# Optimization experiments

Measured on AMD Instinct MI355X. Metric: run time of the kernel, lower is better.

The kernel has to match this reference:

```python
import jax, jax.numpy as jnp
import numpy as np
import math

IN_C, N_EMBD, HEADS = 256, 512, 8

def setup_inputs() -> dict:
    key = jax.random.key(0)
    ks = jax.random.split(key, 5)
    B, T = 64, 500
    x = jax.random.normal(ks[0], (B, T, IN_C), dtype=jnp.float32)
    # torch Linear: y = x @ W.T + b; store W as [out, in]
    w_attn = jax.random.normal(ks[1], (3 * N_EMBD, IN_C), dtype=jnp.float32) * (1.0 / math.sqrt(IN_C))
    b_attn = jax.random.normal(ks[2], (3 * N_EMBD,), dtype=jnp.float32) * 0.02
    w_proj = jax.random.normal(ks[3], (N_EMBD, N_EMBD), dtype=jnp.float32) * (1.0 / math.sqrt(N_EMBD))
    b_proj = jax.random.normal(ks[4], (N_EMBD,), dtype=jnp.float32) * 0.02
    return {"x": x, "w_attn": w_attn, "b_attn": b_attn, "w_proj": w_proj, "b_proj": b_proj}

def reference(x, w_attn, b_attn, w_proj, b_proj):
    B, T, C = x.shape
    H, D = HEADS, N_EMBD // HEADS
    qkv = jnp.einsum('btc,ec->bte', x, w_attn) + b_attn  # [B,T,3*n_embd]
    q, k, v = jnp.split(qkv, 3, axis=-1)
    # [B,T,n_embd] -> [B,H,T,D]
    q = q.reshape(B, T, H, D).transpose(0, 2, 1, 3)
    k = k.reshape(B, T, H, D).transpose(0, 2, 1, 3)
    v = v.reshape(B, T, H, D).transpose(0, 2, 1, 3)
    att = jnp.einsum('bhtd,bhsd->bhts', q, k) * (1.0 / math.sqrt(D))
    # bias buffer is all-ones: masked_fill(bias==0, -inf) is a no-op
    att = jax.nn.softmax(att, axis=-1)
    y = jnp.einsum('bhts,bhsd->bhtd', att, v)  # [B,H,T,D]
    y = y.transpose(0, 2, 1, 3).reshape(B, T, N_EMBD)
    return jnp.einsum('bte,fe->btf', y, w_proj) + b_proj
```

## Files before the change

kernel.cpp:

```cpp
#include <hip/hip_runtime.h>

typedef _Float16 f16;
typedef _Float16 f16x8 __attribute__((ext_vector_type(8)));
typedef _Float16 f16x4 __attribute__((ext_vector_type(4)));
typedef _Float16 f16x2 __attribute__((ext_vector_type(2)));
typedef float    f32x16 __attribute__((ext_vector_type(16)));
typedef unsigned int u32;

typedef const __attribute__((address_space(1))) void GVOID;
typedef __attribute__((address_space(3))) void LVOID;

static __device__ __forceinline__ f32x16 mfma32(f16x8 a, f16x8 b, f32x16 c) {
  return __builtin_amdgcn_mfma_f32_32x32x16_f16(a, b, c, 0, 0, 0);
}
static __device__ __forceinline__ void gl_lds16(const f16* g, f16* l) {
  __builtin_amdgcn_global_load_lds((GVOID*)g, (LVOID*)l, 16, 0, 0);
}
static __device__ __forceinline__ u32 pk(float a, float b) {
  union { f16x2 h; u32 w; } u;
  u.h[0] = (f16)a; u.h[1] = (f16)b;
  return u.w;
}
static __device__ __forceinline__ u32 pkh(f16 a, f16 b) {
  union { f16x2 h; u32 w; } u;
  u.h[0] = a; u.h[1] = b;
  return u.w;
}
static __device__ __forceinline__ f16x8 mkfrag(float a0, float a1, float a2, float a3,
                                               float a4, float a5, float a6, float a7) {
  u32 c01 = pk(a0, a1), c23 = pk(a2, a3), c45 = pk(a4, a5), c67 = pk(a6, a7);
  asm("v_permlane32_swap_b32 %0, %1" : "+v"(c01), "+v"(c45));
  asm("v_permlane32_swap_b32 %0, %1" : "+v"(c23), "+v"(c67));
  union { f16x8 h; u32 w[4]; } u;
  u.w[0] = c01; u.w[1] = c23; u.w[2] = c45; u.w[3] = c67;
  return u.h;
}

__global__ __launch_bounds__(256)
void cvt_all(const float* __restrict__ x,  f16* __restrict__ xh,
             const float* __restrict__ wa, f16* __restrict__ wah,
             const float* __restrict__ wp, f16* __restrict__ wph) {
  int i = (blockIdx.x * 256 + threadIdx.x) * 8;
  const float* s; f16* d;
  if (i < 8192000)            { s = x + i;                 d = xh + i; }
  else if (i < 8192000+393216){ int j = i - 8192000;       s = wa + j; d = wah + j; }
  else                        { int j = i - 8585216;       s = wp + j; d = wph + j; }
  float4 v0 = *(const float4*)(s);
  float4 v1 = *(const float4*)(s + 4);
  f16x8 h;
  h[0] = (f16)v0.x; h[1] = (f16)v0.y; h[2] = (f16)v0.z; h[3] = (f16)v0.w;
  h[4] = (f16)v1.x; h[5] = (f16)v1.y; h[6] = (f16)v1.z; h[7] = (f16)v1.w;
  *(f16x8*)d = h;
}

template<int EPI, int KD, int NDIM>
__global__ __launch_bounds__(512)
void gemmdb(const f16* __restrict__ A, const f16* __restrict__ B,
            const float* __restrict__ bias, f16* __restrict__ outH,
            float* __restrict__ outF) {
  constexpr int KT = KD / 64;
  constexpr int ABUF = 128 * 64, BUFSZ = 2 * ABUF;
  __shared__ __align__(16) f16 lds[2 * BUFSZ];

  const int nwg = gridDim.x, orig = blockIdx.x;
  const int xcd = orig & 7, loc = orig >> 3;
  const int qq = nwg >> 3, rr8 = nwg & 7;
  const int gb = (xcd < rr8 ? xcd * (qq + 1) : rr8 * (qq + 1) + (xcd - rr8) * qq) + loc;
  constexpr int NB = NDIM / 128;
  const int mb = gb / NB, nb = gb - mb * NB;
  const int m0 = mb * 128, n0 = nb * 128;

  const int tid = threadIdx.x, wid = tid >> 6;
  const int l31 = tid & 31, hi = (tid >> 5) & 1;
  const int wm = (wid >> 2) * 64, wn = (wid & 3) * 32;

  f32x16 acc[2] = {};

  const int c0 = tid, c1 = 512 + tid;
  const int r0 = c0 >> 3, col0 = 8 * ((c0 & 7) ^ (r0 & 7));
  const int r1 = c1 >> 3, col1 = 8 * ((c1 & 7) ^ (r1 & 7));

  auto STAGE = [&](int t, int bufi) {
    const int k0 = t * 64;
    f16* Ab = &lds[bufi * BUFSZ];
    f16* Bb = Ab + ABUF;
    gl_lds16(A + (size_t)(m0 + r0) * KD + k0 + col0, &Ab[c0 * 8]);
    gl_lds16(A + (size_t)(m0 + r1) * KD + k0 + col1, &Ab[c1 * 8]);
    gl_lds16(B + (size_t)(n0 + r0) * KD + k0 + col0, &Bb[c0 * 8]);
    gl_lds16(B + (size_t)(n0 + r1) * KD + k0 + col1, &Bb[c1 * 8]);
  };

  STAGE(0, 0);
  int cur = 0;
#pragma unroll
  for (int t = 0; t < KT; ++t) {
    if (t + 1 < KT) {
      STAGE(t + 1, cur ^ 1);
      asm volatile("s_waitcnt vmcnt(4)" ::: "memory");
    } else {
      asm volatile("s_waitcnt vmcnt(0)" ::: "memory");
    }
    __builtin_amdgcn_sched_barrier(0);
    __builtin_amdgcn_s_barrier();

    const f16* Ab = &lds[cur * BUFSZ];
    const f16* Bb = Ab + ABUF;
    __builtin_amdgcn_s_setprio(1);
#pragma unroll
    for (int kk = 0; kk < 4; ++kk) {
      int rb = wn + l31;
      f16x8 bf = *(const f16x8*)&Bb[rb * 64 + 8 * ((2 * kk + hi) ^ (rb & 7))];
      int ra0 = wm + l31, ra1 = wm + 32 + l31;
      f16x8 af0 = *(const f16x8*)&Ab[ra0 * 64 + 8 * ((2 * kk + hi) ^ (ra0 & 7))];
      f16x8 af1 = *(const f16x8*)&Ab[ra1 * 64 + 8 * ((2 * kk + hi) ^ (ra1 & 7))];
      acc[0] = mfma32(af0, bf, acc[0]);
      acc[1] = mfma32(af1, bf, acc[1]);
    }
    __builtin_amdgcn_s_setprio(0);
    __builtin_amdgcn_s_barrier();
    cur ^= 1;
  }

  float bv = bias[n0 + wn + l31];
#pragma unroll
  for (int ms = 0; ms < 2; ++ms)
#pragma unroll
    for (int r = 0; r < 16; ++r) {
      int mrow = (r & 3) + 8 * (r >> 2) + 4 * hi;
      int m_g = m0 + wm + ms * 32 + mrow;
      int n_g = n0 + wn + l31;
      float v = acc[ms][r] + bv;
      if (EPI == 0) outH[(size_t)m_g * NDIM + n_g] = (f16)v;
      else          outF[(size_t)m_g * NDIM + n_g] = v;
    }
}

__global__ __launch_bounds__(512, 4)
void attn_kern(const f16* __restrict__ qkv, f16* __restrict__ Yg) {
  __shared__ __align__(16) f16 Kl[2][64 * 64];
  __shared__ __align__(16) f16 VT[2][64 * 64];
  const int id = blockIdx.x;
  const int g = (id & 7) * 128 + (id >> 3);
  const int bh = g >> 1, qt = g & 1;
  const int b = bh >> 3, h = bh & 7;
  const int tid = threadIdx.x, w = tid >> 6;
  const int l31 = tid & 31, hi = (tid & 63) >> 5, e7 = l31 & 7;

  const f16* base  = qkv + (size_t)b * 500 * 1536 + h * 64;
  const f16* Kbase = base + 512;
  const f16* Vbase = base + 1024;

  const int q = qt * 256 + w * 32 + l31;
  const int qc = q < 500 ? q : 499;
  f16x8 qf[4];
  const f16* qp = base + (size_t)qc * 1536 + hi * 8;
#pragma unroll
  for (int ds = 0; ds < 4; ++ds) qf[ds] = *(const f16x8*)(qp + 16 * ds);
  const f16 qs = (f16)(0.125f * 1.44269504f);
#pragma unroll
  for (int ds = 0; ds < 4; ++ds)
#pragma unroll
    for (int j = 0; j < 8; ++j) qf[ds][j] *= qs;

  f32x16 O0 = {}, O1 = {};
  float l = 0.f;

  const int krow = tid >> 3, kcol = 8 * ((tid & 7) ^ (krow & 7));
  const int kvp = (tid & 31) * 2, d4 = (tid >> 5) * 4;
  f16x4 va, vb;
  const f16x4 VZ4 = {};

  {
    gl_lds16(Kbase + (size_t)krow * 1536 + kcol, &Kl[0][tid * 8]);
    const f16* vp0 = Vbase + (size_t)kvp * 1536 + d4;
    va = *(const f16x4*)vp0; vb = *(const f16x4*)(vp0 + 1536);
#pragma unroll
    for (int dd = 0; dd < 4; ++dd) {
      int d = d4 + dd;
      *(u32*)&VT[0][d * 64 + (kvp ^ ((d & 7) << 3))] = pkh(va[dd], vb[dd]);
    }
    __syncthreads();
  }

#pragma unroll 2
  for (int kt = 0; kt < 8; ++kt) {
    const int cur = kt & 1, nxt = cur ^ 1;
    if (kt < 7) {
      const int kvn = (kt + 1) * 64;
      int kr = kvn + krow; kr = kr < 500 ? kr : 499;
      gl_lds16(Kbase + (size_t)kr * 1536 + kcol, &Kl[nxt][tid * 8]);
      int kv = kvn + kvp;
      int kc0 = kv < 500 ? kv : 499, kc1 = kv + 1 < 500 ? kv + 1 : 499;
      va = *(const f16x4*)(Vbase + (size_t)kc0 * 1536 + d4);
      vb = *(const f16x4*)(Vbase + (size_t)kc1 * 1536 + d4);
      if (kv >= 500) va = VZ4;
      if (kv + 1 >= 500) vb = VZ4;
    }

    f32x16 s0 = {}, s1 = {};
    __builtin_amdgcn_s_setprio(1);
#pragma unroll
    for (int ds = 0; ds < 4; ++ds) {
      f16x8 k0 = *(const f16x8*)&Kl[cur][l31 * 64 + 8 * ((hi + 2 * ds) ^ e7)];
      f16x8 k1 = *(const f16x8*)&Kl[cur][(32 + l31) * 64 + 8 * ((hi + 2 * ds) ^ e7)];
      s0 = mfma32(k0, qf[ds], s0);
      s1 = mfma32(k1, qf[ds], s1);
    }
    __builtin_amdgcn_s_setprio(0);

    if (kt == 7) {
#pragma unroll
      for (int r = 0; r < 16; ++r) {
        int kvL = (r & 3) + 8 * (r >> 2) + 4 * hi;
        if (480 + kvL >= 500) s1[r] = -1e30f;
      }
    }

    float ps = 0.f;
#pragma unroll
    for (int r = 0; r < 16; ++r) {
      float t = __builtin_amdgcn_exp2f(s0[r]);
      s0[r] = t; ps += t;
    }
#pragma unroll
    for (int r = 0; r < 16; ++r) {
      float t = __builtin_amdgcn_exp2f(s1[r]);
      s1[r] = t; ps += t;
    }
    ps += __shfl_xor(ps, 32);
    l += ps;

    f16x8 pf0 = mkfrag(s0[0], s0[1], s0[2], s0[3], s0[4], s0[5], s0[6], s0[7]);
    f16x8 pf1 = mkfrag(s0[8], s0[9], s0[10], s0[11], s0[12], s0[13], s0[14], s0[15]);
    f16x8 pf2 = mkfrag(s1[0], s1[1], s1[2], s1[3], s1[4], s1[5], s1[6], s1[7]);
    f16x8 pf3 = mkfrag(s1[8], s1[9], s1[10], s1[11], s1[12], s1[13], s1[14], s1[15]);

    __builtin_amdgcn_s_setprio(1);
#pragma unroll
    for (int ks = 0; ks < 4; ++ks) {
      f16x8 pf = ks == 0 ? pf0 : ks == 1 ? pf1 : ks == 2 ? pf2 : pf3;
      int sw = (16 * ks + 8 * hi) ^ (e7 << 3);
      f16x8 v0 = *(const f16x8*)&VT[cur][l31 * 64 + sw];
      f16x8 v1 = *(const f16x8*)&VT[cur][(32 + l31) * 64 + sw];
      O0 = mfma32(pf, v0, O0);
      O1 = mfma32(pf, v1, O1);
    }
    __builtin_amdgcn_s_setprio(0);

    if (kt < 7) {
#pragma unroll
      for (int dd = 0; dd < 4; ++dd) {
        int d = d4 + dd;
        *(u32*)&VT[nxt][d * 64 + (kvp ^ ((d & 7) << 3))] = pkh(va[dd], vb[dd]);
      }
    }
    __syncthreads();
  }

  float linv = __builtin_amdgcn_rcpf(l);
#pragma unroll
  for (int r = 0; r < 16; ++r) {
    int rowv = (r & 3) + 8 * (r >> 2) + 4 * hi;
    float li = __shfl(linv, rowv);
    int t = qt * 256 + w * 32 + rowv;
    if (t < 500) {
      size_t rowb = (size_t)(b * 500 + t) * 512 + h * 64;
      Yg[rowb + l31]      = (f16)(O0[r] * li);
      Yg[rowb + 32 + l31] = (f16)(O1[r] * li);
    }
  }
}

extern "C" void kernel_launch(void* const* d_in, const int* in_sizes, int n_in,
                              void* d_out, int out_size, void* d_ws, size_t ws_size,
                              hipStream_t stream) {
  const float* x      = (const float*)d_in[0];
  const float* w_attn = (const float*)d_in[1];
  const float* b_attn = (const float*)d_in[2];
  const float* w_proj = (const float*)d_in[3];
  const float* b_proj = (const float*)d_in[4];
  float* out = (float*)d_out;

  char* wsp = (char*)d_ws;
  f16* Yg   = (f16*)wsp;
  f16* x_h  = (f16*)wsp;
  f16* qkv  = (f16*)(wsp + 32768000);
  f16* wa_h = (f16*)(wsp + 32768000 + 98304000);
  f16* wp_h = (f16*)(wsp + 32768000 + 98304000 + 786432);
  if (ws_size < 132382720) return;

  cvt_all<<<4320, dim3(256), 0, stream>>>(x, x_h, w_attn, wa_h, w_proj, wp_h);

  gemmdb<0, 256, 1536><<<3000, dim3(512), 0, stream>>>(x_h, wa_h, b_attn, qkv, nullptr);
  attn_kern<<<1024, dim3(512), 0, stream>>>(qkv, Yg);
  gemmdb<1, 512, 512><<<1000, dim3(512), 0, stream>>>(Yg, wp_h, b_proj, nullptr, out);
}
```

Measured before the change: 137.7 us.

## Fuse fp32-to-fp16 input conversion into QKV GEMM with larger M tiles

Drops the separate pass that converted x to fp16. The QKV projection GEMM now loads fp32 x directly through registers, converts it while writing to LDS, and uses 256x128 tiles with register-staged double buffering in place of global_load_lds. This removes one full read and write of the fp16 copy of x plus a launch. In exchange the GEMM reads twice the A bytes and loses the asynchronous direct-to-LDS loads, and its epilogue stores scalar f16 values.

New measurement: 159.2 us. 1.16x slower.

```diff
diff --git a/kernel.cpp b/kernel.cpp
--- a/kernel.cpp
+++ b/kernel.cpp
@@ -37,20 +37,142 @@
 }
 
 __global__ __launch_bounds__(256)
-void cvt_all(const float* __restrict__ x,  f16* __restrict__ xh,
-             const float* __restrict__ wa, f16* __restrict__ wah,
-             const float* __restrict__ wp, f16* __restrict__ wph) {
+void cvt_w(const float* __restrict__ wa, f16* __restrict__ wah,
+           const float* __restrict__ wp, f16* __restrict__ wph) {
   int i = (blockIdx.x * 256 + threadIdx.x) * 8;
   const float* s; f16* d;
-  if (i < 8192000)            { s = x + i;                 d = xh + i; }
-  else if (i < 8192000+393216){ int j = i - 8192000;       s = wa + j; d = wah + j; }
-  else                        { int j = i - 8585216;       s = wp + j; d = wph + j; }
+  if (i < 393216) { s = wa + i; d = wah + i; }
+  else            { int j = i - 393216; s = wp + j; d = wph + j; }
   float4 v0 = *(const float4*)(s);
   float4 v1 = *(const float4*)(s + 4);
   f16x8 h;
   h[0] = (f16)v0.x; h[1] = (f16)v0.y; h[2] = (f16)v0.z; h[3] = (f16)v0.w;
   h[4] = (f16)v1.x; h[5] = (f16)v1.y; h[6] = (f16)v1.z; h[7] = (f16)v1.w;
   *(f16x8*)d = h;
+}
+
+__global__ __launch_bounds__(512)
+void gemm1f(const float* __restrict__ A, const f16* __restrict__ B,
+            const float* __restrict__ bias, f16* __restrict__ outH) {
+  constexpr int KD = 256, KT = 4, NB = 12;
+  constexpr int ABUF = 256 * 64, BBUF = 128 * 64, BUFSZ = ABUF + BBUF;
+  __shared__ __align__(16) f16 lds[2 * BUFSZ];
+
+  const int nwg = gridDim.x, orig = blockIdx.x;
+  const int xcd = orig & 7, loc = orig >> 3;
+  const int qq = nwg >> 3, rr8 = nwg & 7;
+  const int gb = (xcd < rr8 ? xcd * (qq + 1) : rr8 * (qq + 1) + (xcd - rr8) * qq) + loc;
+  const int mb = gb / NB, nb = gb - mb * NB;
+  const int m0 = mb * 256, n0 = nb * 128;
+
+  const int tid = threadIdx.x, wid = tid >> 6;
+  const int l31 = tid & 31, hi = (tid >> 5) & 1;
+  const int wm = (wid >> 1) * 64, wn = (wid & 1) * 64;
+
+  f32x16 acc[2][2] = {};
+
+  float4 ar[4][2];
+  uint4  br[2];
+
+  auto LOADS = [&](int t) {
+    const int k0 = t * 64;
+#pragma unroll
+    for (int i = 0; i < 4; ++i) {
+      int c = i * 512 + tid, row = c >> 3, kc = k0 + 8 * (c & 7);
+      const float* p = A + (size_t)(m0 + row) * KD + kc;
+      ar[i][0] = *(const float4*)p;
+      ar[i][1] = *(const float4*)(p + 4);
+    }
+#pragma unroll
+    for (int i = 0; i < 2; ++i) {
+      int c = i * 512 + tid, row = c >> 3, kc = k0 + 8 * (c & 7);
+      br[i] = *(const uint4*)(B + (size_t)(n0 + row) * KD + kc);
+    }
+  };
+  auto WRITES = [&](int bufi) {
+    f16* Ab = &lds[bufi * BUFSZ];
+    f16* Bb = Ab + ABUF;
+#pragma unroll
+    for (int i = 0; i < 4; ++i) {
+      int c = i * 512 + tid, row = c >> 3;
+      int slot = (c & 7) ^ (row & 7);
+      f16x8 h;
+      h[0] = (f16)ar[i][0].x; h[1] = (f16)ar[i][0].y;
+      h[2] = (f16)ar[i][0].z; h[3] = (f16)ar[i][0].w;
+      h[4] = (f16)ar[i][1].x; h[5] = (f16)ar[i][1].y;
+      h[6] = (f16)ar[i][1].z; h[7] = (f16)ar[i][1].w;
+      *(f16x8*)&Ab[row * 64 + 8 * slot] = h;
+    }
+#pragma unroll
+    for (int i = 0; i < 2; ++i) {
+      int c = i * 512 + tid, row = c >> 3;
+      int slot = (c & 7) ^ (row & 7);
+      *(uint4*)&Bb[row * 64 + 8 * slot] = br[i];
+    }
+  };
+
+  LOADS(0);
+  asm volatile("s_waitcnt vmcnt(0)" ::: "memory");
+  WRITES(0);
+  asm volatile("s_waitcnt lgkmcnt(0)" ::: "memory");
+  __builtin_amdgcn_sched_barrier(0);
+  __builtin_amdgcn_s_barrier();
+  __builtin_amdgcn_sched_barrier(0);
+
+  int cur = 0;
+#pragma unroll
+  for (int t = 0; t < KT; ++t) {
+    if (t + 1 < KT) LOADS(t + 1);
+
+    const f16* Ab = &lds[cur * BUFSZ];
+    const f16* Bb = Ab + ABUF;
+    __builtin_amdgcn_s_setprio(1);
+#pragma unroll
+    for (int kk = 0; kk < 4; ++kk) {
+      f16x8 af[2], bf[2];
+#pragma unroll
+      for (int ns = 0; ns < 2; ++ns) {
+        int rb = wn + ns * 32 + l31;
+        bf[ns] = *(const f16x8*)&Bb[rb * 64 + 8 * ((2 * kk + hi) ^ (rb & 7))];
+      }
+#pragma unroll
+      for (int ms = 0; ms < 2; ++ms) {
+        int ra = wm + ms * 32 + l31;
+        af[ms] = *(const f16x8*)&Ab[ra * 64 + 8 * ((2 * kk + hi) ^ (ra & 7))];
+      }
+#pragma unroll
+      for (int ms = 0; ms < 2; ++ms)
+#pragma unroll
+        for (int ns = 0; ns < 2; ++ns)
+          acc[ms][ns] = mfma32(af[ms], bf[ns], acc[ms][ns]);
+    }
+    __builtin_amdgcn_s_setprio(0);
+
+    if (t + 1 < KT) {
+      asm volatile("s_waitcnt vmcnt(0)" ::: "memory");
+      WRITES(cur ^ 1);
+      asm volatile("s_waitcnt lgkmcnt(0)" ::: "memory");
+    }
+    __builtin_amdgcn_sched_barrier(0);
+    __builtin_amdgcn_s_barrier();
+    __builtin_amdgcn_sched_barrier(0);
+    cur ^= 1;
+  }
+
+  float bv[2];
+#pragma unroll
+  for (int ns = 0; ns < 2; ++ns) bv[ns] = bias[n0 + wn + ns * 32 + l31];
+#pragma unroll
+  for (int ms = 0; ms < 2; ++ms)
+#pragma unroll
+    for (int ns = 0; ns < 2; ++ns)
+#pragma unroll
+      for (int r = 0; r < 16; ++r) {
+        int mrow = (r & 3) + 8 * (r >> 2) + 4 * hi;
+        int m_g = m0 + wm + ms * 32 + mrow;
+        int n_g = n0 + wn + ns * 32 + l31;
+        outH[(size_t)m_g * 1536 + n_g] = (f16)(acc[ms][ns][r] + bv[ns]);
+      }
 }
 
 template<int EPI, int KD, int NDIM>
@@ -283,15 +405,14 @@
 
   char* wsp = (char*)d_ws;
   f16* Yg   = (f16*)wsp;
-  f16* x_h  = (f16*)wsp;
   f16* qkv  = (f16*)(wsp + 32768000);
   f16* wa_h = (f16*)(wsp + 32768000 + 98304000);
   f16* wp_h = (f16*)(wsp + 32768000 + 98304000 + 786432);
   if (ws_size < 132382720) return;
 
-  cvt_all<<<4320, dim3(256), 0, stream>>>(x, x_h, w_attn, wa_h, w_proj, wp_h);
-
-  gemmdb<0, 256, 1536><<<3000, dim3(512), 0, stream>>>(x_h, wa_h, b_attn, qkv, nullptr);
+  cvt_w<<<320, dim3(256), 0, stream>>>(w_attn, wa_h, w_proj, wp_h);
+
+  gemm1f<<<1500, dim3(512), 0, stream>>>(x, wa_h, b_attn, qkv);
   attn_kern<<<1024, dim3(512), 0, stream>>>(qkv, Yg);
   gemmdb<1, 512, 512><<<1000, dim3(512), 0, stream>>>(Yg, wp_h, b_proj, nullptr, out);
 }
```

## Use 256x128 tile GEMM for QKV projection instead of double-buffered 128x128

Applied to the files above, without the earlier changes.

Adds a new single-buffered GEMM kernel with 256x128 output tiles, where each of 8 warps computes a 64x64 sub-tile, and uses it for the QKV projection with half as many workgroups. The larger tile increases operand reuse per LDS load and halves the re-reads of B across M blocks. In exchange it drops the double-buffered pipelining, so global loads are no longer overlapped with MFMA work, and the epilogue still writes element-wise scalar stores.

Result: no change. 135.7 us, median of 2 (-1.4%).

```diff
diff --git a/kernel.cpp b/kernel.cpp
--- a/kernel.cpp
+++ b/kernel.cpp
@@ -55,6 +55,79 @@
 
 template<int EPI, int KD, int NDIM>
 __global__ __launch_bounds__(512)
+void gemm256(const f16* __restrict__ A, const f16* __restrict__ B,
+             const float* __restrict__ bias, f16* __restrict__ outH,
+             float* __restrict__ outF) {
+  constexpr int NB = NDIM / 128;
+  const int nwg = gridDim.x;
+  const int orig = blockIdx.x;
+  const int xcd = orig & 7, loc = orig >> 3;
+  const int qq = nwg >> 3, rr8 = nwg & 7;
+  const int g = (xcd < rr8 ? xcd * (qq + 1) : rr8 * (qq + 1) + (xcd - rr8) * qq) + loc;
+  const int mb = g / NB, nb = g - mb * NB;
+  const int m0 = mb * 256, n0 = nb * 128;
+
+  __shared__ __align__(16) f16 As[256 * 64];
+  __shared__ __align__(16) f16 Bs[128 * 64];
+  const int tid = threadIdx.x, wid = tid >> 6;
+  const int l31 = tid & 31, hi = (tid >> 5) & 1;
+  const int wm = (wid >> 1) * 64, wn = (wid & 1) * 64;
+
+  f32x16 acc[2][2] = {};
+
+  for (int k0 = 0; k0 < KD; k0 += 64) {
+    __syncthreads();
+#pragma unroll
+    for (int i = 0; i < 4; ++i) {
+      int c = i * 512 + tid, row = c >> 3;
+      int col = 8 * ((c & 7) ^ (row & 7));
+      gl_lds16(A + (size_t)(m0 + row) * KD + k0 + col, &As[c * 8]);
+    }
+#pragma unroll
+    for (int i = 0; i < 2; ++i) {
+      int c = i * 512 + tid, row = c >> 3;
+      int col = 8 * ((c & 7) ^ (row & 7));
+      gl_lds16(B + (size_t)(n0 + row) * KD + k0 + col, &Bs[c * 8]);
+    }
+    __syncthreads();
+#pragma unroll
+    for (int kk = 0; kk < 4; ++kk) {
+      f16x8 af[2], bf[2];
+#pragma unroll
+      for (int t = 0; t < 2; ++t) {
+        int ra = wm + t * 32 + l31;
+        af[t] = *(const f16x8*)&As[ra * 64 + 8 * ((2 * kk + hi) ^ (ra & 7))];
+        int rb = wn + t * 32 + l31;
+        bf[t] = *(const f16x8*)&Bs[rb * 64 + 8 * ((2 * kk + hi) ^ (rb & 7))];
+      }
+#pragma unroll
+      for (int ms = 0; ms < 2; ++ms)
+#pragma unroll
+        for (int ns = 0; ns < 2; ++ns)
+          acc[ms][ns] = mfma32(af[ms], bf[ns], acc[ms][ns]);
+    }
+  }
+
+  float bv[2];
+  bv[0] = bias[n0 + wn + l31];
+  bv[1] = bias[n0 + wn + 32 + l31];
+#pragma unroll
+  for (int ms = 0; ms < 2; ++ms)
+#pragma unroll
+    for (int ns = 0; ns < 2; ++ns)
+#pragma unroll
+      for (int r = 0; r < 16; ++r) {
+        int mrow = (r & 3) + 8 * (r >> 2) + 4 * hi;
+        int m_g = m0 + wm + ms * 32 + mrow;
+        int n_g = n0 + wn + ns * 32 + l31;
+        float v = acc[ms][ns][r] + bv[ns];
+        if (EPI == 0) outH[(size_t)m_g * NDIM + n_g] = (f16)v;
+        else          outF[(size_t)m_g * NDIM + n_g] = v;
+      }
+}
+
+template<int EPI, int KD, int NDIM>
+__global__ __launch_bounds__(512)
 void gemmdb(const f16* __restrict__ A, const f16* __restrict__ B,
             const float* __restrict__ bias, f16* __restrict__ outH,
             float* __restrict__ outF) {
@@ -291,7 +364,7 @@
 
   cvt_all<<<4320, dim3(256), 0, stream>>>(x, x_h, w_attn, wa_h, w_proj, wp_h);
 
-  gemmdb<0, 256, 1536><<<3000, dim3(512), 0, stream>>>(x_h, wa_h, b_attn, qkv, nullptr);
+  gemm256<0, 256, 1536><<<1500, dim3(512), 0, stream>>>(x_h, wa_h, b_attn, qkv, nullptr);
   attn_kern<<<1024, dim3(512), 0, stream>>>(qkv, Yg);
   gemmdb<1, 512, 512><<<1000, dim3(512), 0, stream>>>(Yg, wp_h, b_proj, nullptr, out);
 }
```
